# Kernel optimization log

Measured on AMD Instinct MI355X. Metric: run time of the kernel, lower is better.

Reference implementation:

```python
import jax, jax.numpy as jnp
import numpy as np

HIDDEN = 768
FFN = 3072
E = 8
TOP_K = 2


def setup_inputs() -> dict:
    key = jax.random.key(0)
    k_x, k_r, k_w1, k_w2 = jax.random.split(key, 4)
    x = jax.random.normal(k_x, (1, 1024, HIDDEN), dtype=jnp.float32)
    # nn.Linear(hidden, E, bias=False): weight applied as x @ W^T; store as [H, E]
    bound = 1.0 / np.sqrt(HIDDEN)
    router_w = jax.random.uniform(k_r, (HIDDEN, E), minval=-bound, maxval=bound, dtype=jnp.float32)
    w1 = jax.random.normal(k_w1, (E, HIDDEN, FFN), dtype=jnp.float32) * 0.02
    w2 = jax.random.normal(k_w2, (E, FFN, HIDDEN), dtype=jnp.float32) * 0.02
    return {"x": x, "router_w": router_w, "w1": w1, "w2": w2}


def reference(x, router_w, w1, w2):
    B, T, H = x.shape
    xf = x.reshape(-1, H)                                  # [N, H]
    logits = xf @ router_w                                 # [N, E] (eval mode: no noise)
    probs = jax.nn.softmax(logits, axis=-1)
    top_v, top_i = jax.lax.top_k(probs, TOP_K)             # [N, K]
    top_v = top_v / jnp.sum(top_v, axis=-1, keepdims=True)  # renormalize top-k probs
    # Combine top-k weights into a dense per-expert gate; zero gates make the
    # dense per-expert computation mathematically identical to sparse dispatch.
    gates = jnp.sum(jax.nn.one_hot(top_i, E, dtype=xf.dtype) * top_v[..., None], axis=1)  # [N, E]
    h = jax.nn.gelu(jnp.einsum('nh,ehf->enf', xf, w1), approximate=False)  # [E, N, F]
    y = jnp.einsum('enf,efh->enh', h, w2)                  # [E, N, H]
    out = jnp.einsum('ne,enh->nh', gates, y)               # [N, H]
    return out.reshape(B, T, H)
```

## Files before the change

kernel.cpp:

```cpp
#include <hip/hip_runtime.h>
#include <cmath>

#define NTOK 1024
#define HD   768
#define FF   3072
#define NE   8
#define NSLOT (NTOK * 2)
#define BK   64

#define NB_ROUTER 256
#define NU_FFN1   1152
#define KSPLIT    4
#define KSEG      (FF / KSPLIT)
#define NU_FFN2   1152

typedef unsigned short u16;
typedef unsigned int   u32;
typedef __bf16 bf16x8 __attribute__((ext_vector_type(8)));
typedef float  f32x4  __attribute__((ext_vector_type(4)));
typedef u16    u16x8  __attribute__((ext_vector_type(8)));

__device__ __forceinline__ u16 f2bf(float f) {
  union { float f; u32 u; } v; v.f = f;
  u32 r = v.u + 0x7FFFu + ((v.u >> 16) & 1u);
  return (u16)(r >> 16);
}

__device__ __forceinline__ void load16(const void* g, void* l) {
  __builtin_amdgcn_global_load_lds(
      (const __attribute__((address_space(1))) u32*)g,
      (__attribute__((address_space(3))) u32*)l, 16, 0, 0);
}

__device__ __forceinline__ int find_expert(const int* __restrict__ seg,
                                           int mt, int* m0_out) {
  int e = -1, m0 = 0, off = 0;
#pragma unroll
  for (int ee = 0; ee < NE; ++ee) {
    const int T = (seg[NE + ee] + 127) >> 7;
    if (e < 0 && mt < off + T) { e = ee; m0 = (mt - off) << 7; }
    off += T;
  }
  *m0_out = m0;
  return e;
}

__global__ __launch_bounds__(256) void router_kernel(
    const float* __restrict__ x, const float* __restrict__ rw,
    u16* __restrict__ xb, int* __restrict__ ti, float* __restrict__ tg,
    int* __restrict__ tos, float* __restrict__ gos, int* __restrict__ seg,
    int* __restrict__ ctr, float* __restrict__ out)
{
  __shared__ int soff[NE], scnt[NE], spos[NE], lastFlag;
  const int tid  = threadIdx.x;
  const int lane = tid & 63;
  const int wid  = tid >> 6;
  const int bid  = blockIdx.x;

  {
    float4* o4 = (float4*)out;
    const float4 zz = {0.f, 0.f, 0.f, 0.f};
#pragma unroll
    for (int i = 0; i < 3; ++i) o4[(size_t)bid * 768 + i * 256 + tid] = zz;
  }

  const int t = bid * 4 + wid;
  const float* xrow = x + (size_t)t * HD;
  u16* xbrow = xb + (size_t)t * HD;

  float acc[NE] = {};
#pragma unroll
  for (int j = 0; j < 12; ++j) {
    const int h = lane + j * 64;
    const float xv = xrow[h];
    xbrow[h] = f2bf(xv);
    const float4 r0 = *(const float4*)(rw + h * 8);
    const float4 r1 = *(const float4*)(rw + h * 8 + 4);
    acc[0] += xv * r0.x; acc[1] += xv * r0.y;
    acc[2] += xv * r0.z; acc[3] += xv * r0.w;
    acc[4] += xv * r1.x; acc[5] += xv * r1.y;
    acc[6] += xv * r1.z; acc[7] += xv * r1.w;
  }
#pragma unroll
  for (int e = 0; e < NE; ++e) {
    float v = acc[e];
#pragma unroll
    for (int off = 32; off; off >>= 1) v += __shfl_down(v, off, 64);
    acc[e] = v;
  }
  if (lane == 0) {
    float v0 = -1e30f, v1 = -1e30f; int i0 = 0, i1 = 0;
#pragma unroll
    for (int e = 0; e < NE; ++e) {
      const float p = acc[e];
      if (p > v0) { v1 = v0; i1 = i0; v0 = p; i0 = e; }
      else if (p > v1) { v1 = p; i1 = e; }
    }
    const float e1 = expf(v1 - v0);
    ti[2 * t] = i0;      ti[2 * t + 1] = i1;
    tg[2 * t] = 1.0f / (1.0f + e1);
    tg[2 * t + 1] = e1 / (1.0f + e1);
  }

  __syncthreads();
  __threadfence();
  if (tid == 0) lastFlag = (atomicAdd(&ctr[1], 1) == NB_ROUTER - 1);
  __syncthreads();
  if (!lastFlag) return;
  __threadfence();

  if (tid < NE) scnt[tid] = 0;
  __syncthreads();
  int mye[8]; float myg[8];
#pragma unroll
  for (int j = 0; j < 8; ++j) {
    const int s = tid * 8 + j;
    mye[j] = ti[s]; myg[j] = tg[s];
    atomicAdd(&scnt[mye[j]], 1);
  }
  __syncthreads();
  if (tid == 0) {
    int o = 0;
    for (int e = 0; e < NE; ++e) {
      soff[e] = o; seg[e] = o; seg[NE + e] = scnt[e]; o += scnt[e];
    }
    ctr[1] = 0;
  }
  if (tid < NE) spos[tid] = 0;
  __syncthreads();
#pragma unroll
  for (int j = 0; j < 8; ++j) {
    const int s = tid * 8 + j;
    const int p = atomicAdd(&spos[mye[j]], 1);
    const int o = soff[mye[j]] + p;
    tos[o] = s >> 1;
    gos[o] = myg[j];
  }
}


#define LOADB(BSRC, BN, K0, D) do {                                          \
  _Pragma("unroll")                                                          \
  for (int j = 0; j < 4; ++j)                                                \
    D[j] = *(const f32x4*)((BSRC) + (size_t)((K0) + rr * 4 + j) * (BN));     \
} while (0)

#define WRITEB(D) do {                                                       \
  _Pragma("unroll")                                                          \
  for (int i = 0; i < 4; ++i) {                                              \
    uint2 w;                                                                 \
    w.x = (u32)f2bf(D[0][i]) | ((u32)f2bf(D[1][i]) << 16);                   \
    w.y = (u32)f2bf(D[2][i]) | ((u32)f2bf(D[3][i]) << 16);                   \
    *(uint2*)(&Bs[wofs[i]]) = w;                                             \
  }                                                                          \
} while (0)

__global__ __launch_bounds__(256) void ffn1_kernel(
    const u16* __restrict__ xb, const float* __restrict__ w1,
    const int* __restrict__ tos, const int* __restrict__ seg,
    u16* __restrict__ hbuf)
{
  const int fid = blockIdx.x;
  const int mt = fid / 48, nt = fid % 48;
  int m0;
  const int e = find_expert(seg, mt, &m0);
  if (e < 0) return;
  const int cnt   = seg[NE + e];
  const int start = seg[e];
  const int n0    = nt * 64;
  const float* w1e = w1 + (size_t)e * HD * FF;

  __shared__ __align__(16) u16 As[128 * 64];
  __shared__ __align__(16) u16 Bs[64 * 64];
  __shared__ int toks[128];

  const int tid = threadIdx.x;
  if (tid < 128) toks[tid] = tos[start + min(m0 + tid, cnt - 1)];
  __syncthreads();

  const int lane = tid & 63;
  const int wid  = tid >> 6;
  const int rsub = lane >> 3;
  const int c8   = (lane & 7) ^ rsub;

  const u16* ag[4]; u16* al[4];
#pragma unroll
  for (int i = 0; i < 4; ++i) {
    const int rb = wid * 8 + i * 32;
    ag[i] = xb + (size_t)toks[rb + rsub] * HD + c8 * 8;
    al[i] = As + rb * 64;
  }

  const int rr = tid >> 4;
  const int cc = (tid & 15) << 2;
  const float* bsrc = w1e + n0 + cc;
  int wofs[4];
#pragma unroll
  for (int i = 0; i < 4; ++i) {
    const int n = cc + i;
    wofs[i] = n * 64 + (((rr >> 1) ^ (n & 7)) << 3) + ((rr & 1) << 2);
  }

  const int wm  = (wid >> 1) << 6;
  const int wn  = (wid & 1) << 5;
  const int q   = lane >> 4;
  const int r16 = lane & 15;

  f32x4 acc[4][2] = {};
  f32x4 breg[2][4];

  LOADB(bsrc, FF, 0, breg[0]);
#pragma unroll
  for (int kk = 0; kk < 12; ++kk) {
    const int k0 = kk * BK;
#pragma unroll
    for (int i = 0; i < 4; ++i) load16(ag[i] + k0, al[i]);
    WRITEB(breg[kk & 1]);
    __syncthreads();
    if (kk < 11) {
      LOADB(bsrc, FF, k0 + BK, breg[(kk + 1) & 1]);
      __builtin_amdgcn_sched_barrier(0);
    }
#pragma unroll
    for (int s = 0; s < 2; ++s) {
      const int pa = ((s << 2) + q) ^ (r16 & 7);
      bf16x8 af[4], bf[2];
#pragma unroll
      for (int t = 0; t < 4; ++t)
        af[t] = *(const bf16x8*)(&As[(wm + t * 16 + r16) * 64 + pa * 8]);
#pragma unroll
      for (int t = 0; t < 2; ++t)
        bf[t] = *(const bf16x8*)(&Bs[(wn + t * 16 + r16) * 64 + pa * 8]);
#pragma unroll
      for (int t = 0; t < 4; ++t)
#pragma unroll
        for (int c = 0; c < 2; ++c)
          acc[t][c] = __builtin_amdgcn_mfma_f32_16x16x32_bf16(af[t], bf[c], acc[t][c], 0, 0, 0);
    }
    __syncthreads();
  }

#pragma unroll
  for (int t = 0; t < 4; ++t) {
    const int mbase = m0 + wm + t * 16 + q * 4;
#pragma unroll
    for (int i = 0; i < 4; ++i) {
      if (mbase + i < cnt) {
        u16* drow = hbuf + (size_t)(start + mbase + i) * FF + n0 + wn;
#pragma unroll
        for (int c = 0; c < 2; ++c) {
          float vv = acc[t][c][i];
          vv = 0.5f * vv * (1.0f + erff(vv * 0.70710678118f));
          drow[c * 16 + r16] = f2bf(vv);
        }
      }
    }
  }
}

__global__ __launch_bounds__(256) void ffn2_kernel(
    const u16* __restrict__ hbuf, const float* __restrict__ w2,
    const int* __restrict__ tos, const float* __restrict__ gos,
    const int* __restrict__ seg, float* __restrict__ out)
{
  const int u    = blockIdx.x;
  const int mt   = u / 48;
  const int rest = u % 48;
  const int n0   = (rest >> 2) * 64;
  const int ks   = rest & 3;
  int m0;
  const int e = find_expert(seg, mt, &m0);
  if (e < 0) return;
  const int cnt   = seg[NE + e];
  const int start = seg[e];
  const int kbase = ks * KSEG;
  const float* w2e = w2 + (size_t)e * FF * HD;

  __shared__ __align__(16) u16 As[128 * 64];
  __shared__ __align__(16) u16 Bs[64 * 64];
  __shared__ int   toks[128];
  __shared__ float gates[128];

  const int tid = threadIdx.x;
  if (tid < 128) {
    const int idx = start + min(m0 + tid, cnt - 1);
    toks[tid]  = tos[idx];
    gates[tid] = gos[idx];
  }
  __syncthreads();

  const int lane = tid & 63;
  const int wid  = tid >> 6;
  const int rsub = lane >> 3;
  const int c8   = (lane & 7) ^ rsub;

  const u16* ag[4]; u16* al[4];
#pragma unroll
  for (int i = 0; i < 4; ++i) {
    const int rb = wid * 8 + i * 32;
    ag[i] = hbuf + (size_t)(start + min(m0 + rb + rsub, cnt - 1)) * FF + kbase + c8 * 8;
    al[i] = As + rb * 64;
  }

  const int rr = tid >> 4;
  const int cc = (tid & 15) << 2;
  const float* bsrc = w2e + (size_t)kbase * HD + n0 + cc;
  int wofs[4];
#pragma unroll
  for (int i = 0; i < 4; ++i) {
    const int n = cc + i;
    wofs[i] = n * 64 + (((rr >> 1) ^ (n & 7)) << 3) + ((rr & 1) << 2);
  }

  const int wm  = (wid >> 1) << 6;
  const int wn  = (wid & 1) << 5;
  const int q   = lane >> 4;
  const int r16 = lane & 15;

  f32x4 acc[4][2] = {};
  f32x4 breg[2][4];

  LOADB(bsrc, HD, 0, breg[0]);
#pragma unroll
  for (int kk = 0; kk < 12; ++kk) {
    const int k0 = kk * BK;
#pragma unroll
    for (int i = 0; i < 4; ++i) load16(ag[i] + k0, al[i]);
    WRITEB(breg[kk & 1]);
    __syncthreads();
    if (kk < 11) {
      LOADB(bsrc, HD, k0 + BK, breg[(kk + 1) & 1]);
      __builtin_amdgcn_sched_barrier(0);
    }
#pragma unroll
    for (int s = 0; s < 2; ++s) {
      const int pa = ((s << 2) + q) ^ (r16 & 7);
      bf16x8 af[4], bf[2];
#pragma unroll
      for (int t = 0; t < 4; ++t)
        af[t] = *(const bf16x8*)(&As[(wm + t * 16 + r16) * 64 + pa * 8]);
#pragma unroll
      for (int t = 0; t < 2; ++t)
        bf[t] = *(const bf16x8*)(&Bs[(wn + t * 16 + r16) * 64 + pa * 8]);
#pragma unroll
      for (int t = 0; t < 4; ++t)
#pragma unroll
        for (int c = 0; c < 2; ++c)
          acc[t][c] = __builtin_amdgcn_mfma_f32_16x16x32_bf16(af[t], bf[c], acc[t][c], 0, 0, 0);
    }
    __syncthreads();
  }

#pragma unroll
  for (int t = 0; t < 4; ++t) {
    const int mbase = wm + t * 16 + q * 4;
#pragma unroll
    for (int i = 0; i < 4; ++i) {
      const int mloc = mbase + i;
      if (m0 + mloc < cnt) {
        const int tok  = toks[mloc];
        const float gv = gates[mloc];
        float* drow = out + (size_t)tok * HD + n0 + wn;
#pragma unroll
        for (int c = 0; c < 2; ++c)
          atomicAdd(drow + c * 16 + r16, gv * acc[t][c][i]);
      }
    }
  }
}

extern "C" void kernel_launch(void* const* d_in, const int* in_sizes, int n_in,
                              void* d_out, int out_size, void* d_ws, size_t ws_size,
                              hipStream_t stream) {
  const float* x  = (const float*)d_in[0];
  const float* rw = (const float*)d_in[1];
  const float* w1 = (const float*)d_in[2];
  const float* w2 = (const float*)d_in[3];
  float* out = (float*)d_out;

  char* ws = (char*)d_ws;
  const size_t o_xb    = 0;
  const size_t o_hbuf  = o_xb + (size_t)NTOK * HD * 2;
  const size_t o_tos   = o_hbuf + (size_t)NSLOT * FF * 2;
  const size_t o_gos   = o_tos + (size_t)NSLOT * 4;
  const size_t o_seg   = o_gos + (size_t)NSLOT * 4;
  const size_t o_ctr   = o_seg + 64 * 4;
  const size_t o_ti    = o_ctr + 64;
  const size_t o_tg    = o_ti + (size_t)NSLOT * 4;
  u16*   xb    = (u16*)(ws + o_xb);
  u16*   hbuf  = (u16*)(ws + o_hbuf);
  int*   tos   = (int*)(ws + o_tos);
  float* gos   = (float*)(ws + o_gos);
  int*   seg   = (int*)(ws + o_seg);
  int*   ctr   = (int*)(ws + o_ctr);
  int*   ti    = (int*)(ws + o_ti);
  float* tg    = (float*)(ws + o_tg);

  hipMemsetAsync(ctr, 0, 64, stream);
  hipLaunchKernelGGL(router_kernel, dim3(NB_ROUTER), dim3(256), 0, stream,
                     x, rw, xb, ti, tg, tos, gos, seg, ctr, out);
  hipLaunchKernelGGL(ffn1_kernel, dim3(NU_FFN1), dim3(256), 0, stream,
                     xb, w1, tos, seg, hbuf);
  hipLaunchKernelGGL(ffn2_kernel, dim3(NU_FFN2), dim3(256), 0, stream,
                     hbuf, w2, tos, gos, seg, out);
}
```

Before: 266.0 us.

## Shrink M tile to 64 and double-buffer LDS in both expert GEMMs

Reduces the per-block M tile from 128 to 64 rows, which raises the block count (39 M-tiles) and cuts padding waste for uneven expert segments. Adds double-buffered A/B LDS tiles with a two-deep register prefetch of fp32 weights, so only one barrier per K step is needed and loads overlap the MFMA work. Also changes the weight load pattern to float2 rows, with a new swizzle for the B tile. Each weight tile is now reused by fewer tokens, so total weight traffic from global memory grows.

```diff
diff --git a/kernel.cpp b/kernel.cpp
--- a/kernel.cpp
+++ b/kernel.cpp
@@ -9,10 +9,11 @@
 #define BK   64
 
 #define NB_ROUTER 256
-#define NU_FFN1   1152
+#define NU_MT     39
+#define NU_FFN1   (NU_MT * 48)
 #define KSPLIT    4
 #define KSEG      (FF / KSPLIT)
-#define NU_FFN2   1152
+#define NU_FFN2   (NU_MT * 12 * KSPLIT)
 
 typedef unsigned short u16;
 typedef unsigned int   u32;
@@ -37,8 +38,8 @@
   int e = -1, m0 = 0, off = 0;
 #pragma unroll
   for (int ee = 0; ee < NE; ++ee) {
-    const int T = (seg[NE + ee] + 127) >> 7;
-    if (e < 0 && mt < off + T) { e = ee; m0 = (mt - off) << 7; }
+    const int T = (seg[NE + ee] + 63) >> 6;
+    if (e < 0 && mt < off + T) { e = ee; m0 = (mt - off) << 6; }
     off += T;
   }
   *m0_out = m0;
@@ -139,19 +140,38 @@
 }
 
 
-#define LOADB(BSRC, BN, K0, D) do {                                          \
+#define LOADB(SRC, LDN, K0, B) do {                                          \
   _Pragma("unroll")                                                          \
-  for (int j = 0; j < 4; ++j)                                                \
-    D[j] = *(const f32x4*)((BSRC) + (size_t)((K0) + rr * 4 + j) * (BN));     \
+  for (int j = 0; j < 8; ++j)                                                \
+    B[j] = *(const float2*)((SRC) + (size_t)((K0) + rr2 * 8 + j) * (LDN));   \
 } while (0)
 
-#define WRITEB(D) do {                                                       \
+#define WRITEB(B, DST) do {                                                  \
+  u16x8 v0, v1;                                                              \
   _Pragma("unroll")                                                          \
-  for (int i = 0; i < 4; ++i) {                                              \
-    uint2 w;                                                                 \
-    w.x = (u32)f2bf(D[0][i]) | ((u32)f2bf(D[1][i]) << 16);                   \
-    w.y = (u32)f2bf(D[2][i]) | ((u32)f2bf(D[3][i]) << 16);                   \
-    *(uint2*)(&Bs[wofs[i]]) = w;                                             \
+  for (int j = 0; j < 8; ++j) { v0[j] = f2bf(B[j].x); v1[j] = f2bf(B[j].y); }\
+  *(u16x8*)((DST) + wof0) = v0;                                              \
+  *(u16x8*)((DST) + wof1) = v1;                                              \
+} while (0)
+
+#define MFMA_STEP(ACUR, BCUR) do {                                           \
+  _Pragma("unroll")                                                          \
+  for (int s = 0; s < 2; ++s) {                                              \
+    const int ca = ((s << 2) + q) ^ (r16 & 7);                               \
+    const int cb = ((s << 2) + q) ^ ((r16 >> 1) & 7);                        \
+    bf16x8 af[2], bf[2];                                                     \
+    _Pragma("unroll")                                                        \
+    for (int t = 0; t < 2; ++t)                                              \
+      af[t] = *(const bf16x8*)(&(ACUR)[(wm + t * 16 + r16) * 64 + ca * 8]);  \
+    _Pragma("unroll")                                                        \
+    for (int c = 0; c < 2; ++c)                                              \
+      bf[c] = *(const bf16x8*)(&(BCUR)[(wn + c * 16 + r16) * 64 + cb * 8]);  \
+    _Pragma("unroll")                                                        \
+    for (int t = 0; t < 2; ++t)                                              \
+      _Pragma("unroll")                                                      \
+      for (int c = 0; c < 2; ++c)                                            \
+        acc[t][c] = __builtin_amdgcn_mfma_f32_16x16x32_bf16(af[t], bf[c],    \
+                                                            acc[t][c], 0, 0, 0); \
   }                                                                          \
 } while (0)
 
@@ -168,14 +188,13 @@
   const int cnt   = seg[NE + e];
   const int start = seg[e];
   const int n0    = nt * 64;
-  const float* w1e = w1 + (size_t)e * HD * FF;
-
-  __shared__ __align__(16) u16 As[128 * 64];
-  __shared__ __align__(16) u16 Bs[64 * 64];
-  __shared__ int toks[128];
+
+  __shared__ __align__(16) u16 As[2][64 * 64];
+  __shared__ __align__(16) u16 Bs[2][64 * 64];
+  __shared__ int toks[64];
 
   const int tid = threadIdx.x;
-  if (tid < 128) toks[tid] = tos[start + min(m0 + tid, cnt - 1)];
+  if (tid < 64) toks[tid] = tos[start + min(m0 + tid, cnt - 1)];
   __syncthreads();
 
   const int lane = tid & 63;
@@ -183,65 +202,54 @@
   const int rsub = lane >> 3;
   const int c8   = (lane & 7) ^ rsub;
 
-  const u16* ag[4]; u16* al[4];
-#pragma unroll
-  for (int i = 0; i < 4; ++i) {
+  const u16* ag[2]; int ao[2];
+#pragma unroll
+  for (int i = 0; i < 2; ++i) {
     const int rb = wid * 8 + i * 32;
     ag[i] = xb + (size_t)toks[rb + rsub] * HD + c8 * 8;
-    al[i] = As + rb * 64;
-  }
-
-  const int rr = tid >> 4;
-  const int cc = (tid & 15) << 2;
-  const float* bsrc = w1e + n0 + cc;
-  int wofs[4];
-#pragma unroll
-  for (int i = 0; i < 4; ++i) {
-    const int n = cc + i;
-    wofs[i] = n * 64 + (((rr >> 1) ^ (n & 7)) << 3) + ((rr & 1) << 2);
-  }
-
-  const int wm  = (wid >> 1) << 6;
+    ao[i] = rb * 64;
+  }
+
+  const int rr2 = tid >> 5;
+  const int np  = tid & 31;
+  const float* bsrc = w1 + (size_t)e * HD * FF + n0 + np * 2;
+  const int wof0 = (np * 2) * 64 + ((rr2 ^ (np & 7)) << 3);
+  const int wof1 = wof0 + 64;
+
+  const int wm  = (wid >> 1) << 5;
   const int wn  = (wid & 1) << 5;
   const int q   = lane >> 4;
   const int r16 = lane & 15;
 
-  f32x4 acc[4][2] = {};
-  f32x4 breg[2][4];
-
-  LOADB(bsrc, FF, 0, breg[0]);
+  f32x4 acc[2][2] = {};
+  float2 breg0[8], breg1[8];
+
+  LOADB(bsrc, FF, 0, breg0);
+  LOADB(bsrc, FF, BK, breg1);
+#pragma unroll
+  for (int i = 0; i < 2; ++i) load16(ag[i], &As[0][ao[i]]);
+  WRITEB(breg0, &Bs[0][0]);
+  __syncthreads();
+
 #pragma unroll
   for (int kk = 0; kk < 12; ++kk) {
-    const int k0 = kk * BK;
-#pragma unroll
-    for (int i = 0; i < 4; ++i) load16(ag[i] + k0, al[i]);
-    WRITEB(breg[kk & 1]);
+    const int cur = kk & 1, nxt = cur ^ 1;
+    if (kk + 2 < 12) {
+      if (cur == 0) LOADB(bsrc, FF, (kk + 2) * BK, breg0);
+      else          LOADB(bsrc, FF, (kk + 2) * BK, breg1);
+    }
+    if (kk + 1 < 12) {
+#pragma unroll
+      for (int i = 0; i < 2; ++i) load16(ag[i] + (kk + 1) * BK, &As[nxt][ao[i]]);
+      if (nxt == 0) WRITEB(breg0, &Bs[0][0]);
+      else          WRITEB(breg1, &Bs[1][0]);
+    }
+    MFMA_STEP(As[cur], Bs[cur]);
     __syncthreads();
-    if (kk < 11) {
-      LOADB(bsrc, FF, k0 + BK, breg[(kk + 1) & 1]);
-      __builtin_amdgcn_sched_barrier(0);
-    }
-#pragma unroll
-    for (int s = 0; s < 2; ++s) {
-      const int pa = ((s << 2) + q) ^ (r16 & 7);
-      bf16x8 af[4], bf[2];
-#pragma unroll
-      for (int t = 0; t < 4; ++t)
-        af[t] = *(const bf16x8*)(&As[(wm + t * 16 + r16) * 64 + pa * 8]);
-#pragma unroll
-      for (int t = 0; t < 2; ++t)
-        bf[t] = *(const bf16x8*)(&Bs[(wn + t * 16 + r16) * 64 + pa * 8]);
-#pragma unroll
-      for (int t = 0; t < 4; ++t)
-#pragma unroll
-        for (int c = 0; c < 2; ++c)
-          acc[t][c] = __builtin_amdgcn_mfma_f32_16x16x32_bf16(af[t], bf[c], acc[t][c], 0, 0, 0);
-    }
-    __syncthreads();
-  }
-
-#pragma unroll
-  for (int t = 0; t < 4; ++t) {
+  }
+
+#pragma unroll
+  for (int t = 0; t < 2; ++t) {
     const int mbase = m0 + wm + t * 16 + q * 4;
 #pragma unroll
     for (int i = 0; i < 4; ++i) {
@@ -274,15 +282,14 @@
   const int cnt   = seg[NE + e];
   const int start = seg[e];
   const int kbase = ks * KSEG;
-  const float* w2e = w2 + (size_t)e * FF * HD;
-
-  __shared__ __align__(16) u16 As[128 * 64];
-  __shared__ __align__(16) u16 Bs[64 * 64];
-  __shared__ int   toks[128];
-  __shared__ float gates[128];
+
+  __shared__ __align__(16) u16 As[2][64 * 64];
+  __shared__ __align__(16) u16 Bs[2][64 * 64];
+  __shared__ int   toks[64];
+  __shared__ float gates[64];
 
   const int tid = threadIdx.x;
-  if (tid < 128) {
+  if (tid < 64) {
     const int idx = start + min(m0 + tid, cnt - 1);
     toks[tid]  = tos[idx];
     gates[tid] = gos[idx];
@@ -294,65 +301,54 @@
   const int rsub = lane >> 3;
   const int c8   = (lane & 7) ^ rsub;
 
-  const u16* ag[4]; u16* al[4];
-#pragma unroll
-  for (int i = 0; i < 4; ++i) {
+  const u16* ag[2]; int ao[2];
+#pragma unroll
+  for (int i = 0; i < 2; ++i) {
     const int rb = wid * 8 + i * 32;
     ag[i] = hbuf + (size_t)(start + min(m0 + rb + rsub, cnt - 1)) * FF + kbase + c8 * 8;
-    al[i] = As + rb * 64;
-  }
-
-  const int rr = tid >> 4;
-  const int cc = (tid & 15) << 2;
-  const float* bsrc = w2e + (size_t)kbase * HD + n0 + cc;
-  int wofs[4];
-#pragma unroll
-  for (int i = 0; i < 4; ++i) {
-    const int n = cc + i;
-    wofs[i] = n * 64 + (((rr >> 1) ^ (n & 7)) << 3) + ((rr & 1) << 2);
-  }
-
-  const int wm  = (wid >> 1) << 6;
+    ao[i] = rb * 64;
+  }
+
+  const int rr2 = tid >> 5;
+  const int np  = tid & 31;
+  const float* bsrc = w2 + (size_t)e * FF * HD + (size_t)kbase * HD + n0 + np * 2;
+  const int wof0 = (np * 2) * 64 + ((rr2 ^ (np & 7)) << 3);
+  const int wof1 = wof0 + 64;
+
+  const int wm  = (wid >> 1) << 5;
   const int wn  = (wid & 1) << 5;
   const int q   = lane >> 4;
   const int r16 = lane & 15;
 
-  f32x4 acc[4][2] = {};
-  f32x4 breg[2][4];
-
-  LOADB(bsrc, HD, 0, breg[0]);
+  f32x4 acc[2][2] = {};
+  float2 breg0[8], breg1[8];
+
+  LOADB(bsrc, HD, 0, breg0);
+  LOADB(bsrc, HD, BK, breg1);
+#pragma unroll
+  for (int i = 0; i < 2; ++i) load16(ag[i], &As[0][ao[i]]);
+  WRITEB(breg0, &Bs[0][0]);
+  __syncthreads();
+
 #pragma unroll
   for (int kk = 0; kk < 12; ++kk) {
-    const int k0 = kk * BK;
-#pragma unroll
-    for (int i = 0; i < 4; ++i) load16(ag[i] + k0, al[i]);
-    WRITEB(breg[kk & 1]);
+    const int cur = kk & 1, nxt = cur ^ 1;
+    if (kk + 2 < 12) {
+      if (cur == 0) LOADB(bsrc, HD, (kk + 2) * BK, breg0);
+      else          LOADB(bsrc, HD, (kk + 2) * BK, breg1);
+    }
+    if (kk + 1 < 12) {
+#pragma unroll
+      for (int i = 0; i < 2; ++i) load16(ag[i] + (kk + 1) * BK, &As[nxt][ao[i]]);
+      if (nxt == 0) WRITEB(breg0, &Bs[0][0]);
+      else          WRITEB(breg1, &Bs[1][0]);
+    }
+    MFMA_STEP(As[cur], Bs[cur]);
     __syncthreads();
-    if (kk < 11) {
-      LOADB(bsrc, HD, k0 + BK, breg[(kk + 1) & 1]);
-      __builtin_amdgcn_sched_barrier(0);
-    }
-#pragma unroll
-    for (int s = 0; s < 2; ++s) {
-      const int pa = ((s << 2) + q) ^ (r16 & 7);
-      bf16x8 af[4], bf[2];
-#pragma unroll
-      for (int t = 0; t < 4; ++t)
-        af[t] = *(const bf16x8*)(&As[(wm + t * 16 + r16) * 64 + pa * 8]);
-#pragma unroll
-      for (int t = 0; t < 2; ++t)
-        bf[t] = *(const bf16x8*)(&Bs[(wn + t * 16 + r16) * 64 + pa * 8]);
-#pragma unroll
-      for (int t = 0; t < 4; ++t)
-#pragma unroll
-        for (int c = 0; c < 2; ++c)
-          acc[t][c] = __builtin_amdgcn_mfma_f32_16x16x32_bf16(af[t], bf[c], acc[t][c], 0, 0, 0);
-    }
-    __syncthreads();
-  }
-
-#pragma unroll
-  for (int t = 0; t < 4; ++t) {
+  }
+
+#pragma unroll
+  for (int t = 0; t < 2; ++t) {
     const int mbase = wm + t * 16 + q * 4;
 #pragma unroll
     for (int i = 0; i < 4; ++i) {
```

Measured after the change: 255.8 us. -3.8%, faster.
